# Performance work log

Hardware: AMD Instinct MI355X
Metric: run time of the kernel (lower is better)

Reference implementation:

```python
import jax, jax.numpy as jnp
import numpy as np
from itertools import combinations

NUM_LAGS = 9
WINDOWS = 4
HIDDEN = 256
BS = 32768
EPS = 1e-5  # BatchNorm eps


def _mean_adj():
    # Reconstruct the fixed per-sample DGL graph from get_batch_graph and
    # fold mean-aggregation into a row-normalized dense 9x9 matrix
    # (duplicate edges across overlapping windows count with multiplicity,
    # exactly as DGL's mailbox mean does).
    edges = []
    for j in range(WINDOWS, NUM_LAGS + 1):
        t = list(range(j - WINDOWS, j))
        combs = list(combinations(t, 2))
        for e in combs[:-1]:  # code drops the last combination per window
            edges.append(e)
    edges.append((NUM_LAGS - 2, NUM_LAGS - 1))
    edges.append((NUM_LAGS - 1, 0))
    A = np.zeros((NUM_LAGS, NUM_LAGS), np.float32)
    for s, d in edges:
        A[d, s] += 1.0  # messages flow src -> dst
    deg = A.sum(axis=1, keepdims=True)
    return A / np.maximum(deg, 1.0)

_A = jnp.asarray(_mean_adj())  # [9, 9]


def setup_inputs() -> dict:
    key = jax.random.key(0)
    ks = jax.random.split(key, 12)
    H = HIDDEN
    s = lambda fan_in: 1.0 / np.sqrt(fan_in)
    return {
        "lags": jax.random.normal(ks[0], (BS, NUM_LAGS), jnp.float32),
        "weather": jax.random.normal(ks[1], (BS, NUM_LAGS, 8), jnp.float32),
        "W_l1": jax.random.normal(ks[2], (1, H), jnp.float32) * s(1),
        "b_l1": jnp.zeros((H,), jnp.float32),
        "g_bn": jnp.ones((H,), jnp.float32),
        "b_bn": jnp.zeros((H,), jnp.float32),
        "W_l2": jax.random.normal(ks[3], (H, H), jnp.float32) * s(H),
        "b_l2": jnp.zeros((H,), jnp.float32),
        "W_w1": jax.random.normal(ks[4], (8, H), jnp.float32) * s(8),
        "b_w1": jnp.zeros((H,), jnp.float32),
        "W_w2": jax.random.normal(ks[5], (H, H), jnp.float32) * s(H),
        "b_w2": jnp.zeros((H,), jnp.float32),
        "Wm1": jax.random.normal(ks[6], (2 * H, H), jnp.float32) * s(2 * H),
        "bm1": jnp.zeros((H,), jnp.float32),
        "Wm2": jax.random.normal(ks[7], (2 * H, H), jnp.float32) * s(2 * H),
        "bm2": jnp.zeros((H,), jnp.float32),
        "W_reg": jax.random.normal(ks[8], (NUM_LAGS * H, 1), jnp.float32) * s(NUM_LAGS * H),
        "b_reg": jnp.zeros((1,), jnp.float32),
    }


def reference(lags, weather, W_l1, b_l1, g_bn, b_bn, W_l2, b_l2,
              W_w1, b_w1, W_w2, b_w2, Wm1, bm1, Wm2, bm2, W_reg, b_reg):
    bs = lags.shape[0]
    # lags branch: Linear(1,H) -> tanh -> [dropout=id] -> eval BatchNorm -> Linear(H,H) -> tanh
    l = jnp.tanh(lags.reshape(-1, 1) @ W_l1 + b_l1)
    l = l * (g_bn / jnp.sqrt(1.0 + EPS)) + b_bn  # BN eval: running_mean=0, running_var=1
    l = jnp.tanh(l @ W_l2 + b_l2)
    # weather branch: Linear(8,H) -> tanh -> Linear(H,H) -> tanh
    w = jnp.tanh(weather.reshape(-1, 8) @ W_w1 + b_w1)
    w = jnp.tanh(w @ W_w2 + b_w2)
    l = l.reshape(bs, NUM_LAGS, -1)
    w = w.reshape(bs, NUM_LAGS, -1)
    # Two MGN layers: mean-aggregate neighbor l and w, concat, linear merge.
    for Wm, bm in ((Wm1, bm1), (Wm2, bm2)):
        ml = jnp.einsum('ds,bsh->bdh', _A, l)  # mean over mailbox 'l'
        mw = jnp.einsum('ds,bsh->bdh', _A, w)  # mean over mailbox 'w'
        l = jnp.concatenate([ml, mw], axis=-1) @ Wm + bm
        w = mw
    hg = l.reshape(bs, -1)  # [bs, 9*H]
    return hg @ W_reg + b_reg
```

## Files before the change

kernel.cpp:

```cpp
#include <hip/hip_runtime.h>

typedef __attribute__((ext_vector_type(8))) short short8;
typedef __attribute__((ext_vector_type(4))) float float4v;

#define NLAGS 9
#define HID 256
#define GSAMP 16
#define NTHREADS 1024
#define SBUF_SHORTS (36864 + 512 + 288)

#define NK 2048
#define LUT_STRIDE 2056
#define SLO -8.0f
#define KINV 128.0f

union S8 { short8 v; unsigned short u[8]; };

__device__ __forceinline__ unsigned short f2b(float f) {
  union { float f; unsigned int i; } c; c.f = f;
  return (unsigned short)((c.i + 0x7FFFu + ((c.i >> 16) & 1u)) >> 16);
}
__device__ __forceinline__ float sane(float x) {
  return (__builtin_isfinite(x) && fabsf(x) < 1e30f) ? x : 0.0f;
}
__device__ __forceinline__ unsigned int pkbf16(float lo, float hi) {
  unsigned int r;
  asm("v_cvt_pk_bf16_f32 %0, %1, %2" : "=v"(r) : "v"(lo), "v"(hi));
  return r;
}
__device__ __forceinline__ float ftanh(float x) {
  float t = __expf(2.0f * x);
  return 1.0f - 2.0f * __builtin_amdgcn_rcpf(t + 1.0f);
}
__device__ __forceinline__ float4v mfma16(short8 a, short8 b, float4v c) {
  return __builtin_amdgcn_mfma_f32_16x16x32_bf16(a, b, c, 0, 0, 0);
}

__device__ __forceinline__ int tmC(int row, int c) {
  int base = ((row >> 4) * 8 + (c >> 2)) * 512 + (row & 15) * 32 + (c & 3) * 8;
  return base ^ ((((c >> 2) ^ (row >> 2)) & 3) << 4);
}
__device__ __forceinline__ int tmE(int row, int col) {
  int base = ((row >> 4) * 8 + (col >> 5)) * 512 + (row & 15) * 32 + (col & 31);
  return base ^ ((((col >> 5) ^ (row >> 2)) & 3) << 4);
}

#define A_TABLE { \
    {0,0,0,0,0,0,0,0,1}, \
    {1,0,0,0,0,0,0,0,0}, \
    {1.f/3,2.f/3,0,0,0,0,0,0,0}, \
    {0.2f,0.4f,0.4f,0,0,0,0,0,0}, \
    {0,0.2f,0.4f,0.4f,0,0,0,0,0}, \
    {0,0,0.2f,0.4f,0.4f,0,0,0,0}, \
    {0,0,0,0.2f,0.4f,0.4f,0,0,0}, \
    {0,0,0,0,0.25f,0.5f,0.25f,0,0}, \
    {0,0,0,0,0,1.f/3,1.f/3,1.f/3,0}, \
  }

__global__ void prep_all(const float* __restrict__ Ww2,
                         const float* __restrict__ Ww1,
                         const float* __restrict__ Wm2,
                         const float* __restrict__ Wreg,
                         const float* __restrict__ bm2,
                         const float* __restrict__ breg,
                         unsigned short* __restrict__ ws,
                         float* __restrict__ vtab)
{
  const int b = blockIdx.x;
  if (b < 144) {
    int idx = b * 512 + threadIdx.x + 65536;
    if (idx < 131072) {
      int j = idx - 65536; int n = j >> 8, k = j & 255;
      ws[idx] = f2b(sane(Ww2[k * 256 + n]));
    } else {
      int j = idx - 131072; int n = j >> 5, k = j & 31;
      ws[idx] = (k < 8) ? f2b(sane(Ww1[k * 256 + n])) : (unsigned short)0;
    }
    return;
  }
  const float A[9][9] = A_TABLE;
  const int lane = threadIdx.x & 63;
  const int g = (b - 144) * 8 + (threadIdx.x >> 6);
  if (g < 4608) {
    int mat = (g >= 2304);
    int w = g - mat * 2304;
    int d = w >> 8, k = w & 255;
    float coef[9];
    #pragma unroll
    for (int dp = 0; dp < 9; ++dp) {
      if (!mat) {
        coef[dp] = A[dp][d];
      } else {
        float s = 0.f;
        #pragma unroll
        for (int e = 0; e < 9; ++e) s += A[dp][e] * A[e][d];
        coef[dp] = s;
      }
    }
    const float* wm2row = Wm2 + (size_t)(mat * 256 + k) * 256;
    float acc = 0.f;
    #pragma unroll
    for (int it = 0; it < 4; ++it) {
      int h = lane + it * 64;
      float wp = 0.f;
      #pragma unroll
      for (int dp = 0; dp < 9; ++dp) wp = fmaf(coef[dp], Wreg[dp * 256 + h], wp);
      acc = fmaf(wp, wm2row[h], acc);
    }
    #pragma unroll
    for (int off = 32; off >= 1; off >>= 1) acc += __shfl_down(acc, off);
    if (lane == 0) vtab[5120 + g] = acc;
  } else if (g == 4608) {
    float c0 = 0.f;
    #pragma unroll
    for (int it = 0; it < 4; ++it) {
      int h = lane + it * 64;
      float cs = 0.f;
      #pragma unroll
      for (int d = 0; d < 9; ++d) cs += Wreg[d * 256 + h];
      c0 = fmaf(bm2[h], cs, c0);
    }
    #pragma unroll
    for (int off = 32; off >= 1; off >>= 1) c0 += __shfl_down(c0, off);
    if (lane == 0) vtab[9728] = c0 + breg[0];
  }
}

__global__ void prep2b_kernel(const float* __restrict__ Wm1,
                              const float* __restrict__ bm1,
                              float* __restrict__ vtab)
{
  const float A[9][9] = A_TABLE;
  const float* V1s = vtab + 5120;
  const float* V2s = vtab + 7424;
  const int lane = threadIdx.x & 63;
  const int g = blockIdx.x * 8 + (threadIdx.x >> 6);
  if (g < 4608) {
    int mat = (g >= 2304);
    int w = g - mat * 2304;
    int s = w >> 8, k = w & 255;
    const float* wm1row = Wm1 + (size_t)(mat * 256 + k) * 256;
    float acc = 0.f;
    #pragma unroll
    for (int it = 0; it < 4; ++it) {
      int h = lane + it * 64;
      float u = 0.f;
      #pragma unroll
      for (int d = 0; d < 9; ++d) u = fmaf(A[d][s], V1s[d * 256 + h], u);
      acc = fmaf(u, wm1row[h], acc);
    }
    #pragma unroll
    for (int off = 32; off >= 1; off >>= 1) acc += __shfl_down(acc, off);
    if (lane == 0) vtab[g] = acc + (mat ? V2s[s * 256 + k] : 0.f);
  } else if (g == 4608) {
    float c = 0.f;
    #pragma unroll
    for (int it = 0; it < 4; ++it) {
      int h = lane + it * 64;
      float vs = 0.f;
      #pragma unroll
      for (int d = 0; d < 9; ++d) vs += V1s[d * 256 + h];
      c = fmaf(bm1[h], vs, c);
    }
    #pragma unroll
    for (int off = 32; off >= 1; off >>= 1) c += __shfl_down(c, off);
    if (lane == 0) vtab[4608] = c + vtab[9728];
  }
}

__global__ void prep3_lut(const float* __restrict__ Wl1,
                          const float* __restrict__ bl1,
                          const float* __restrict__ gbn,
                          const float* __restrict__ bbn,
                          const float* __restrict__ Wl2,
                          const float* __restrict__ bl2,
                          const float* __restrict__ vtab,
                          float* __restrict__ lutf)
{
  __shared__ float l0s[2][256];
  __shared__ float red[2][9][4];
  const int tid = threadIdx.x;
  const int b = blockIdx.x;
  const float BNS = 0.99999500003750f;
  {
    float w = Wl1[tid], a = bl1[tid], g = gbn[tid] * BNS, q = bbn[tid];
    #pragma unroll
    for (int j = 0; j < 2; ++j) {
      float s = SLO + (float)(b * 2 + j) * 0.0078125f;
      l0s[j][tid] = fmaf(ftanh(fmaf(s, w, a)), g, q);
    }
  }
  __syncthreads();
  float z0 = bl2[tid], z1 = z0;
  #pragma unroll 8
  for (int k = 0; k < 256; ++k) {
    float wv = Wl2[k * 256 + tid];
    z0 = fmaf(l0s[0][k], wv, z0);
    z1 = fmaf(l0s[1][k], wv, z1);
  }
  float t0 = ftanh(z0), t1 = ftanh(z1);
  const int lane = tid & 63, w4 = tid >> 6;
  for (int d = 0; d < 9; ++d) {
    float T1h = vtab[d * 256 + tid];
    float v0 = t0 * T1h, v1 = t1 * T1h;
    #pragma unroll
    for (int off = 32; off >= 1; off >>= 1) {
      v0 += __shfl_down(v0, off);
      v1 += __shfl_down(v1, off);
    }
    if (lane == 0) { red[0][d][w4] = v0; red[1][d][w4] = v1; }
  }
  __syncthreads();
  if (tid < 18) {
    int j = tid / 9, d = tid - j * 9;
    float v = red[j][d][0] + red[j][d][1] + red[j][d][2] + red[j][d][3];
    lutf[d * LUT_STRIDE + (b * 2 + j)] = v;
  }
}

__global__ void __launch_bounds__(NTHREADS, 2)
fused_kernel(const float* __restrict__ lags,
             const float* __restrict__ weather,
             const float* __restrict__ bw1,
             const float* __restrict__ bw2,
             const unsigned short* __restrict__ ws,
             const float* __restrict__ vtab,
             float* __restrict__ out)
{
  __shared__ __align__(16) unsigned short sBuf[SBUF_SHORTS];
  unsigned short* sT = sBuf;
  float* scratch  = (float*)(sBuf + 36864);
  float* scratch2 = (float*)(sBuf + 36864 + 512);

  const int tid = threadIdx.x;
  const int wave = tid >> 6;
  const int lane16 = tid & 15;
  const int g4 = (tid >> 4) & 3;
  const int s0 = blockIdx.x * GSAMP;

  const float* lutf = (const float*)ws;
  const unsigned short* Ww2t = ws + 65536;
  const unsigned short* Ww1p = ws + 131072;

  const int c = wave * 16 + lane16;

  if (tid < 144) {
    int samp = tid / 9, d = tid - samp * 9;
    float x = lags[(s0 + samp) * NLAGS + d];
    float tp = (x - SLO) * KINV;
    tp = fminf(fmaxf(tp, 0.0f), (float)(NK - 2) + 0.999f);
    int j = (int)tp; float fr = tp - (float)j;
    const float* row = lutf + d * LUT_STRIDE;
    float lo = row[j], hi = row[j + 1];
    scratch2[tid] = fmaf(fr, hi - lo, lo);
  }

  {
    short8 bf = *(const short8*)(Ww1p + c * 32 + g4 * 8);
    float bia = bw1[c];
    #pragma unroll
    for (int m = 0; m < 9; ++m) {
      S8 a8;
      if (g4 == 0) {
        const float* wp = weather + (size_t)(s0 + lane16) * 72 + m * 8;
        float4v x0 = *(const float4v*)(wp);
        float4v x1 = *(const float4v*)(wp + 4);
        a8.v = (short8){0,0,0,0,0,0,0,0};
        unsigned int p0 = pkbf16(x0[0], x0[1]), p1 = pkbf16(x0[2], x0[3]);
        unsigned int p2 = pkbf16(x1[0], x1[1]), p3 = pkbf16(x1[2], x1[3]);
        a8.u[0] = (unsigned short)p0; a8.u[1] = (unsigned short)(p0 >> 16);
        a8.u[2] = (unsigned short)p1; a8.u[3] = (unsigned short)(p1 >> 16);
        a8.u[4] = (unsigned short)p2; a8.u[5] = (unsigned short)(p2 >> 16);
        a8.u[6] = (unsigned short)p3; a8.u[7] = (unsigned short)(p3 >> 16);
      } else {
        a8.v = (short8){0,0,0,0,0,0,0,0};
      }
      float4v zz = {0.f, 0.f, 0.f, 0.f};
      float4v ac = mfma16(a8.v, bf, zz);
      float t0 = ftanh(ac[0] + bia), t1 = ftanh(ac[1] + bia);
      float t2 = ftanh(ac[2] + bia), t3 = ftanh(ac[3] + bia);
      unsigned int p01 = pkbf16(t0, t1);
      unsigned int p23 = pkbf16(t2, t3);
      int r0 = m * 16 + g4 * 4;
      sT[tmE(r0 + 0, c)] = (unsigned short)p01;
      sT[tmE(r0 + 1, c)] = (unsigned short)(p01 >> 16);
      sT[tmE(r0 + 2, c)] = (unsigned short)p23;
      sT[tmE(r0 + 3, c)] = (unsigned short)(p23 >> 16);
    }
  }
  __syncthreads();

  float P[4] = {0.f, 0.f, 0.f, 0.f};

  {
    float bia = bw2[c];
    #pragma unroll 1
    for (int mg = 0; mg < 3; ++mg) {
      int lz = 0;
      asm volatile("" : "+v"(lz));
      const unsigned short* Wb = Ww2t + lz;
      float4v acc[3];
      #pragma unroll
      for (int mi = 0; mi < 3; ++mi) {
        float4v z = {0.f,0.f,0.f,0.f};
        acc[mi] = z;
      }
      #pragma unroll
      for (int kk = 0; kk < 8; ++kk) {
        short8 b0 = *(const short8*)(Wb + c * 256 + kk * 32 + g4 * 8);
        #pragma unroll
        for (int mi = 0; mi < 3; ++mi) {
          int m = mg * 3 + mi;
          short8 a = *(const short8*)(sT + tmC(m * 16 + lane16, kk * 4 + g4));
          acc[mi] = mfma16(a, b0, acc[mi]);
        }
      }
      #pragma unroll
      for (int mi = 0; mi < 3; ++mi) {
        int m = mg * 3 + mi;
        float twc = vtab[2304 + m * 256 + c];
        #pragma unroll
        for (int i = 0; i < 4; ++i) {
          float t0 = ftanh(acc[mi][i] + bia);
          P[i] = fmaf(t0, twc, P[i]);
        }
      }
    }
  }

  #pragma unroll
  for (int off = 8; off >= 1; off >>= 1) {
    #pragma unroll
    for (int i = 0; i < 4; ++i) P[i] += __shfl_down(P[i], off, 16);
  }
  if (lane16 == 0) {
    #pragma unroll
    for (int i = 0; i < 4; ++i) scratch[wave * 16 + g4 * 4 + i] = P[i];
  }
  __syncthreads();
  if (tid < GSAMP) {
    float sum = 0.f;
    #pragma unroll
    for (int w = 0; w < 16; ++w) sum += scratch[w * 16 + tid];
    float lsum = 0.f;
    #pragma unroll
    for (int d = 0; d < 9; ++d) lsum += scratch2[tid * 9 + d];
    out[s0 + tid] = sum + lsum + vtab[4608];
  }
}

extern "C" void kernel_launch(void* const* d_in, const int* in_sizes, int n_in,
                              void* d_out, int out_size, void* d_ws, size_t ws_size,
                              hipStream_t stream) {
  const float* lags    = (const float*)d_in[0];
  const float* weather = (const float*)d_in[1];
  const float* Wl1     = (const float*)d_in[2];
  const float* bl1     = (const float*)d_in[3];
  const float* gbn     = (const float*)d_in[4];
  const float* bbn     = (const float*)d_in[5];
  const float* Wl2     = (const float*)d_in[6];
  const float* bl2     = (const float*)d_in[7];
  const float* Ww1     = (const float*)d_in[8];
  const float* bw1     = (const float*)d_in[9];
  const float* Ww2     = (const float*)d_in[10];
  const float* bw2     = (const float*)d_in[11];
  const float* Wm1     = (const float*)d_in[12];
  const float* bm1     = (const float*)d_in[13];
  const float* Wm2     = (const float*)d_in[14];
  const float* bm2     = (const float*)d_in[15];
  const float* Wreg    = (const float*)d_in[16];
  const float* breg    = (const float*)d_in[17];
  unsigned short* ws = (unsigned short*)d_ws;
  float* vtab = (float*)(ws + 139264);
  float* lutf = (float*)ws;

  prep_all<<<721, 512, 0, stream>>>(Ww2, Ww1, Wm2, Wreg, bm2, breg, ws, vtab);
  prep2b_kernel<<<577, 512, 0, stream>>>(Wm1, bm1, vtab);
  prep3_lut<<<1024, 256, 0, stream>>>(Wl1, bl1, gbn, bbn, Wl2, bl2, vtab, lutf);

  const int nblocks = 32768 / GSAMP;
  fused_kernel<<<nblocks, NTHREADS, 0, stream>>>(
      lags, weather, bw1, bw2, ws, vtab, (float*)d_out);
}
```

Measured before the change: 233.6 us.

## Make fused kernel persistent: 256 blocks each looping over 8 sample groups

Launches 256 blocks of 1024 threads (launch bounds lowered to one block per CU) instead of one block per 16-sample group. Each block now loops over 8 groups. Per-column biases and regression weights are loaded once and kept in registers, and the lag-LUT scratch is double-buffered. The second GEMM is fully unrolled over all 9 row tiles with 9 accumulators instead of 3 chunks of 3. This is meant to amortise block launch and per-block constant loads, but it lowers resident waves per CU and raises register pressure, which can reduce latency hiding.

```diff
diff --git a/kernel.cpp b/kernel.cpp
--- a/kernel.cpp
+++ b/kernel.cpp
@@ -7,7 +7,9 @@
 #define HID 256
 #define GSAMP 16
 #define NTHREADS 1024
-#define SBUF_SHORTS (36864 + 512 + 288)
+#define NGRP 8
+#define NBLK 256
+#define SBUF_SHORTS (36864 + 512 + 576)
 
 #define NK 2048
 #define LUT_STRIDE 2056
@@ -218,7 +220,7 @@
   }
 }
 
-__global__ void __launch_bounds__(NTHREADS, 2)
+__global__ void __launch_bounds__(NTHREADS, 1)
 fused_kernel(const float* __restrict__ lags,
              const float* __restrict__ weather,
              const float* __restrict__ bw1,
@@ -236,7 +238,6 @@
   const int wave = tid >> 6;
   const int lane16 = tid & 15;
   const int g4 = (tid >> 4) & 3;
-  const int s0 = blockIdx.x * GSAMP;
 
   const float* lutf = (const float*)ws;
   const unsigned short* Ww2t = ws + 65536;
@@ -244,108 +245,110 @@
 
   const int c = wave * 16 + lane16;
 
-  if (tid < 144) {
-    int samp = tid / 9, d = tid - samp * 9;
-    float x = lags[(s0 + samp) * NLAGS + d];
-    float tp = (x - SLO) * KINV;
-    tp = fminf(fmaxf(tp, 0.0f), (float)(NK - 2) + 0.999f);
-    int j = (int)tp; float fr = tp - (float)j;
-    const float* row = lutf + d * LUT_STRIDE;
-    float lo = row[j], hi = row[j + 1];
-    scratch2[tid] = fmaf(fr, hi - lo, lo);
-  }
-
-  {
-    short8 bf = *(const short8*)(Ww1p + c * 32 + g4 * 8);
-    float bia = bw1[c];
-    #pragma unroll
-    for (int m = 0; m < 9; ++m) {
-      S8 a8;
-      if (g4 == 0) {
-        const float* wp = weather + (size_t)(s0 + lane16) * 72 + m * 8;
-        float4v x0 = *(const float4v*)(wp);
-        float4v x1 = *(const float4v*)(wp + 4);
-        a8.v = (short8){0,0,0,0,0,0,0,0};
-        unsigned int p0 = pkbf16(x0[0], x0[1]), p1 = pkbf16(x0[2], x0[3]);
-        unsigned int p2 = pkbf16(x1[0], x1[1]), p3 = pkbf16(x1[2], x1[3]);
-        a8.u[0] = (unsigned short)p0; a8.u[1] = (unsigned short)(p0 >> 16);
-        a8.u[2] = (unsigned short)p1; a8.u[3] = (unsigned short)(p1 >> 16);
-        a8.u[4] = (unsigned short)p2; a8.u[5] = (unsigned short)(p2 >> 16);
-        a8.u[6] = (unsigned short)p3; a8.u[7] = (unsigned short)(p3 >> 16);
-      } else {
-        a8.v = (short8){0,0,0,0,0,0,0,0};
-      }
-      float4v zz = {0.f, 0.f, 0.f, 0.f};
-      float4v ac = mfma16(a8.v, bf, zz);
-      float t0 = ftanh(ac[0] + bia), t1 = ftanh(ac[1] + bia);
-      float t2 = ftanh(ac[2] + bia), t3 = ftanh(ac[3] + bia);
-      unsigned int p01 = pkbf16(t0, t1);
-      unsigned int p23 = pkbf16(t2, t3);
-      int r0 = m * 16 + g4 * 4;
-      sT[tmE(r0 + 0, c)] = (unsigned short)p01;
-      sT[tmE(r0 + 1, c)] = (unsigned short)(p01 >> 16);
-      sT[tmE(r0 + 2, c)] = (unsigned short)p23;
-      sT[tmE(r0 + 3, c)] = (unsigned short)(p23 >> 16);
-    }
-  }
-  __syncthreads();
-
-  float P[4] = {0.f, 0.f, 0.f, 0.f};
-
-  {
-    float bia = bw2[c];
-    #pragma unroll 1
-    for (int mg = 0; mg < 3; ++mg) {
-      int lz = 0;
-      asm volatile("" : "+v"(lz));
-      const unsigned short* Wb = Ww2t + lz;
-      float4v acc[3];
-      #pragma unroll
-      for (int mi = 0; mi < 3; ++mi) {
+  const short8 bf = *(const short8*)(Ww1p + c * 32 + g4 * 8);
+  const float bia1v = bw1[c];
+  const float bia2v = bw2[c];
+  float twc[9];
+  #pragma unroll
+  for (int m = 0; m < 9; ++m) twc[m] = vtab[2304 + m * 256 + c];
+  const float c0p = vtab[4608];
+
+  #pragma unroll 1
+  for (int it = 0; it < NGRP; ++it) {
+    const int s0 = (blockIdx.x * NGRP + it) * GSAMP;
+    float* sc2 = scratch2 + (it & 1) * 144;
+
+    if (tid < 144) {
+      int samp = tid / 9, d = tid - samp * 9;
+      float x = lags[(s0 + samp) * NLAGS + d];
+      float tp = (x - SLO) * KINV;
+      tp = fminf(fmaxf(tp, 0.0f), (float)(NK - 2) + 0.999f);
+      int j = (int)tp; float fr = tp - (float)j;
+      const float* row = lutf + d * LUT_STRIDE;
+      float lo = row[j], hi = row[j + 1];
+      sc2[tid] = fmaf(fr, hi - lo, lo);
+    }
+
+    {
+      #pragma unroll
+      for (int m = 0; m < 9; ++m) {
+        S8 a8;
+        if (g4 == 0) {
+          const float* wp = weather + (size_t)(s0 + lane16) * 72 + m * 8;
+          float4v x0 = *(const float4v*)(wp);
+          float4v x1 = *(const float4v*)(wp + 4);
+          a8.v = (short8){0,0,0,0,0,0,0,0};
+          unsigned int p0 = pkbf16(x0[0], x0[1]), p1 = pkbf16(x0[2], x0[3]);
+          unsigned int p2 = pkbf16(x1[0], x1[1]), p3 = pkbf16(x1[2], x1[3]);
+          a8.u[0] = (unsigned short)p0; a8.u[1] = (unsigned short)(p0 >> 16);
+          a8.u[2] = (unsigned short)p1; a8.u[3] = (unsigned short)(p1 >> 16);
+          a8.u[4] = (unsigned short)p2; a8.u[5] = (unsigned short)(p2 >> 16);
+          a8.u[6] = (unsigned short)p3; a8.u[7] = (unsigned short)(p3 >> 16);
+        } else {
+          a8.v = (short8){0,0,0,0,0,0,0,0};
+        }
+        float4v zz = {0.f, 0.f, 0.f, 0.f};
+        float4v ac = mfma16(a8.v, bf, zz);
+        float t0 = ftanh(ac[0] + bia1v), t1 = ftanh(ac[1] + bia1v);
+        float t2 = ftanh(ac[2] + bia1v), t3 = ftanh(ac[3] + bia1v);
+        unsigned int p01 = pkbf16(t0, t1);
+        unsigned int p23 = pkbf16(t2, t3);
+        int r0 = m * 16 + g4 * 4;
+        sT[tmE(r0 + 0, c)] = (unsigned short)p01;
+        sT[tmE(r0 + 1, c)] = (unsigned short)(p01 >> 16);
+        sT[tmE(r0 + 2, c)] = (unsigned short)p23;
+        sT[tmE(r0 + 3, c)] = (unsigned short)(p23 >> 16);
+      }
+    }
+    __syncthreads();
+
+    float P[4] = {0.f, 0.f, 0.f, 0.f};
+
+    {
+      float4v acc[9];
+      #pragma unroll
+      for (int m = 0; m < 9; ++m) {
         float4v z = {0.f,0.f,0.f,0.f};
-        acc[mi] = z;
+        acc[m] = z;
       }
       #pragma unroll
       for (int kk = 0; kk < 8; ++kk) {
-        short8 b0 = *(const short8*)(Wb + c * 256 + kk * 32 + g4 * 8);
+        short8 b0 = *(const short8*)(Ww2t + c * 256 + kk * 32 + g4 * 8);
         #pragma unroll
-        for (int mi = 0; mi < 3; ++mi) {
-          int m = mg * 3 + mi;
+        for (int m = 0; m < 9; ++m) {
           short8 a = *(const short8*)(sT + tmC(m * 16 + lane16, kk * 4 + g4));
-          acc[mi] = mfma16(a, b0, acc[mi]);
+          acc[m] = mfma16(a, b0, acc[m]);
         }
       }
       #pragma unroll
-      for (int mi = 0; mi < 3; ++mi) {
-        int m = mg * 3 + mi;
-        float twc = vtab[2304 + m * 256 + c];
+      for (int m = 0; m < 9; ++m) {
         #pragma unroll
         for (int i = 0; i < 4; ++i) {
-          float t0 = ftanh(acc[mi][i] + bia);
-          P[i] = fmaf(t0, twc, P[i]);
+          float t0 = ftanh(acc[m][i] + bia2v);
+          P[i] = fmaf(t0, twc[m], P[i]);
         }
       }
     }
-  }
-
-  #pragma unroll
-  for (int off = 8; off >= 1; off >>= 1) {
-    #pragma unroll
-    for (int i = 0; i < 4; ++i) P[i] += __shfl_down(P[i], off, 16);
-  }
-  if (lane16 == 0) {
-    #pragma unroll
-    for (int i = 0; i < 4; ++i) scratch[wave * 16 + g4 * 4 + i] = P[i];
-  }
-  __syncthreads();
-  if (tid < GSAMP) {
-    float sum = 0.f;
-    #pragma unroll
-    for (int w = 0; w < 16; ++w) sum += scratch[w * 16 + tid];
-    float lsum = 0.f;
-    #pragma unroll
-    for (int d = 0; d < 9; ++d) lsum += scratch2[tid * 9 + d];
-    out[s0 + tid] = sum + lsum + vtab[4608];
+
+    #pragma unroll
+    for (int off = 8; off >= 1; off >>= 1) {
+      #pragma unroll
+      for (int i = 0; i < 4; ++i) P[i] += __shfl_down(P[i], off, 16);
+    }
+    if (lane16 == 0) {
+      #pragma unroll
+      for (int i = 0; i < 4; ++i) scratch[wave * 16 + g4 * 4 + i] = P[i];
+    }
+    __syncthreads();
+    if (tid < GSAMP) {
+      float sum = 0.f;
+      #pragma unroll
+      for (int w = 0; w < 16; ++w) sum += scratch[w * 16 + tid];
+      float lsum = 0.f;
+      #pragma unroll
+      for (int d = 0; d < 9; ++d) lsum += sc2[tid * 9 + d];
+      out[s0 + tid] = sum + lsum + c0p;
+    }
   }
 }
 
@@ -378,7 +381,6 @@
   prep2b_kernel<<<577, 512, 0, stream>>>(Wm1, bm1, vtab);
   prep3_lut<<<1024, 256, 0, stream>>>(Wl1, bl1, gbn, bbn, Wl2, bl2, vtab, lutf);
 
-  const int nblocks = 32768 / GSAMP;
-  fused_kernel<<<nblocks, NTHREADS, 0, stream>>>(
+  fused_kernel<<<NBLK, NTHREADS, 0, stream>>>(
       lags, weather, bw1, bw2, ws, vtab, (float*)d_out);
 }
```

Measured after the change: 361.5 us. 54.7% more time.
